# Kernel tuning notes

Measured on AMD Instinct MI355X. Metric: run time of the kernel, lower is better.

Reference implementation:

```python
import jax, jax.numpy as jnp
import numpy as np

B = 64       # number of graphs (regular batching)
NPER = 2048  # nodes per graph
K = 16       # kNN neighbors (includes self, as torch_cluster.knn does)
D_IN = 64
D_OUT = 64


def setup_inputs() -> dict:
    key = jax.random.key(0)
    k1, k2 = jax.random.split(key, 2)
    x = jax.random.normal(k1, (B * NPER, D_IN), jnp.float32)
    batch = jnp.repeat(jnp.arange(B, dtype=jnp.int32), NPER)
    # MLP: Linear(2*in_channels, out_channels, bias=True) + ReLU
    weight = jax.random.normal(k2, (D_OUT, 2 * D_IN), jnp.float32) * (1.0 / np.sqrt(2 * D_IN))
    bias = jnp.zeros((D_OUT,), jnp.float32)
    return {"x": x, "batch": batch, "weight": weight, "bias": bias}


def reference(x, batch, weight, bias):
    # batch is a regular assignment (NPER nodes per graph) -> block the kNN per graph
    d = x.shape[1]
    xb = x.reshape(B, NPER, d)                                   # [B, n, d]
    # squared euclidean distances within each graph
    sq = jnp.sum(xb * xb, axis=-1)                               # [B, n]
    dist = sq[:, :, None] + sq[:, None, :] - 2.0 * jnp.einsum('bnd,bmd->bnm', xb, xb)
    # k nearest (smallest distance); self-distance 0 -> self included, matching PyG knn
    _, idx = jax.lax.top_k(-dist, K)                             # [B, n, K]
    xj = jax.vmap(lambda feats, ids: feats[ids])(xb, idx)        # [B, n, K, d]
    xi = xb[:, :, None, :]                                        # [B, n, 1, d]
    msg = jnp.concatenate([jnp.broadcast_to(xi, xj.shape), xj - xi], axis=-1)  # [B,n,K,2d]
    h = jax.nn.relu(jnp.einsum('bnkf,of->bnko', msg, weight) + bias)
    out = jnp.max(h, axis=2)                                      # max aggregation over neighbors
    return out.reshape(B * NPER, -1)
```

## Files before the change

### kernel.cpp

```cpp
#include <hip/hip_runtime.h>
#include <cfloat>

#define BB 64
#define NPERB 2048
#define KNN 16
#define NTOT (BB*NPERB)
#define NCAND 24

typedef __bf16 bf16x8 __attribute__((ext_vector_type(8)));
typedef float  f32x4  __attribute__((ext_vector_type(4)));

__device__ __forceinline__ unsigned int med3u(unsigned int a, unsigned int b, unsigned int c) {
    unsigned int d;
    asm("v_med3_u32 %0, %1, %2, %3" : "=v"(d) : "v"(a), "v"(b), "v"(c));
    return d;
}

__device__ __forceinline__ float np_sq64(const float* __restrict__ xs) {
    float r[8];
#pragma unroll
    for (int j = 0; j < 8; ++j) r[j] = __fmul_rn(xs[j], xs[j]);
#pragma unroll
    for (int i = 1; i < 8; ++i)
#pragma unroll
        for (int j = 0; j < 8; ++j)
            r[j] = __fadd_rn(r[j], __fmul_rn(xs[8*i + j], xs[8*i + j]));
    float t01 = __fadd_rn(r[0], r[1]);
    float t23 = __fadd_rn(r[2], r[3]);
    float t45 = __fadd_rn(r[4], r[5]);
    float t67 = __fadd_rn(r[6], r[7]);
    return __fadd_rn(__fadd_rn(t01, t23), __fadd_rn(t45, t67));
}

__device__ __forceinline__ unsigned short bf16rn(float f) {
    unsigned int u = __float_as_uint(f);
    u += 0x7fffu + ((u >> 16) & 1u);
    return (unsigned short)(u >> 16);
}
__device__ __forceinline__ unsigned int pk2(float a, float b) {
    return ((unsigned int)bf16rn(b) << 16) | (unsigned int)bf16rn(a);
}

__global__ __launch_bounds__(256) void k_transform(const float* __restrict__ x,
    const float* __restrict__ w, const float* __restrict__ bias,
    float* __restrict__ Aout, float* __restrict__ Bvv, float* __restrict__ sqnp,
    unsigned int* __restrict__ xbu)
{
    __shared__ float w1m[64*64];
    __shared__ float w2t[64*64];
    __shared__ float xs[128*64];
    int t = threadIdx.x;
    int r0 = blockIdx.x * 128;
#pragma unroll
    for (int i = 0; i < 16; ++i) {
        int e = t + i*256; int f = e >> 6; int o = e & 63;
        float w2 = w[o*128 + 64 + f];
        float w1 = w[o*128 + f];
        w2t[f*64 + o] = w2;
        w1m[f*64 + o] = w1 - w2;
    }
#pragma unroll
    for (int i = 0; i < 32; ++i) { int idx = t + i*256; xs[idx] = x[(size_t)r0*64 + idx]; }
    __syncthreads();
#pragma unroll
    for (int i = 0; i < 16; ++i) {
        int e = t + i*256;
        xbu[(size_t)r0*32 + e] = pk2(xs[2*e], xs[2*e + 1]);
    }
    int o = t & 63;
    float br = bias[o];
    for (int g = 0; g < 32; ++g) {
        int rl = g*4 + (t >> 6);
        float a1 = 0.f, a2 = 0.f;
#pragma unroll
        for (int f = 0; f < 64; ++f) {
            float xv = xs[rl*64 + f];
            a1 += xv * w1m[f*64 + o];
            a2 += xv * w2t[f*64 + o];
        }
        int row = r0 + rl;
        Aout[(size_t)row*64 + o] = a1 + br;
        Bvv[(size_t)row*64 + o] = a2;
        if (o == 0) sqnp[row] = np_sq64(&xs[rl*64]);
    }
}

__global__ __launch_bounds__(256, 4) void k_topk(const float4* __restrict__ x4,
    const uint4* __restrict__ xb, const float* __restrict__ sq, int* __restrict__ nbr)
{
    __shared__ __align__(16) char smem[28160];
    unsigned short* bsh0 = (unsigned short*)smem;
    unsigned short* bsh1 = (unsigned short*)(smem + 9216);
    unsigned short* rsh  = (unsigned short*)(smem + 18432);
    float* sqc           = (float*)(smem + 27648);
    unsigned int* cand   = (unsigned int*)smem;
    unsigned short* cand24 = (unsigned short*)(smem + 17408);

    int t = threadIdx.x;
    int lane = t & 63;
    int w = t >> 6;
    int ln = lane & 15, qd = lane >> 4;
    int batch = blockIdx.x >> 5;
    int strip = blockIdx.x & 31;
    int rbase = batch * NPERB;
    int r0g = rbase + strip * 64;

    {
        const uint4* src = xb + (size_t)r0g * 8;
#pragma unroll
        for (int i = 0; i < 2; ++i) {
            int l = t + i*256;
            uint4 v = src[l];
            *(uint4*)&rsh[(l >> 3)*72 + (l & 7)*8] = v;
        }
    }
    uint4 pf0, pf1; float sqpf;
    {
        const uint4* src = xb + (size_t)rbase * 8;
        pf0 = src[t]; pf1 = src[t + 256];
        sqpf = (t < 64) ? sq[rbase + t] : 0.f;
    }
    __syncthreads();
    bf16x8 rf0 = *(const bf16x8*)&rsh[(w*16 + ln)*72 + qd*8];
    bf16x8 rf1 = *(const bf16x8*)&rsh[(w*16 + ln)*72 + 32 + qd*8];
    float sqr16 = sq[r0g + w*16 + ln] + 16.f;

    *(uint4*)&bsh0[(t >> 3)*72 + (t & 7)*8] = pf0;
    { int l1 = t + 256; *(uint4*)&bsh0[(l1 >> 3)*72 + (l1 & 7)*8] = pf1; }
    if (t < 64) sqc[t] = sqpf;
    {
        const uint4* src = xb + ((size_t)rbase + 64) * 8;
        pf0 = src[t]; pf1 = src[t + 256];
        sqpf = (t < 64) ? sq[rbase + 64 + t] : 0.f;
    }
    __syncthreads();

    unsigned int ks[16];
#pragma unroll
    for (int j = 0; j < 16; ++j) ks[j] = 0xFFFFFFFFu;

    for (int ct = 0; ct < 32; ++ct) {
        unsigned short* bcur = (ct & 1) ? bsh1 : bsh0;
        const float* sqcur = sqc + (ct & 1)*64;
#pragma unroll
        for (int ct2 = 0; ct2 < 4; ++ct2) {
            int pt = ct2*16 + ln;
            bf16x8 a0 = *(const bf16x8*)&bcur[pt*72 + qd*8];
            bf16x8 a1 = *(const bf16x8*)&bcur[pt*72 + 32 + qd*8];
            f32x4 acc = {0.f, 0.f, 0.f, 0.f};
            acc = __builtin_amdgcn_mfma_f32_16x16x32_bf16(a0, rf0, acc, 0, 0, 0);
            acc = __builtin_amdgcn_mfma_f32_16x16x32_bf16(a1, rf1, acc, 0, 0, 0);
            f32x4 sc4 = *(const f32x4*)&sqcur[ct2*16 + qd*4];
            int idxb = ct*64 + ct2*16 + qd*4;
#pragma unroll
            for (int j = 0; j < 4; ++j) {
                float s = fmaf(-2.f, acc[j], sc4[j] + sqr16);
                unsigned int u = (__float_as_uint(s) & 0xFFFFF800u) | (unsigned int)(idxb + j);
#pragma unroll
                for (int jj = 15; jj >= 1; --jj) ks[jj] = med3u(u, ks[jj-1], ks[jj]);
                ks[0] = min(ks[0], u);
            }
        }
        if (ct < 31) {
            unsigned short* bnext = (ct & 1) ? bsh0 : bsh1;
            *(uint4*)&bnext[(t >> 3)*72 + (t & 7)*8] = pf0;
            { int l1 = t + 256; *(uint4*)&bnext[(l1 >> 3)*72 + (l1 & 7)*8] = pf1; }
            if (t < 64) sqc[((ct + 1) & 1)*64 + t] = sqpf;
            if (ct < 30) {
                const uint4* src = xb + ((size_t)rbase + (ct + 2)*64) * 8;
                pf0 = src[t]; pf1 = src[t + 256];
                sqpf = (t < 64) ? sq[rbase + (ct + 2)*64 + t] : 0.f;
            }
        }
        __syncthreads();
    }

    {
        int r = w*16 + ln;
#pragma unroll
        for (int j = 0; j < 16; ++j) cand[r*68 + qd*16 + j] = ks[j];
    }
    __syncthreads();

    if (t < 64) {
        unsigned int m24[NCAND];
#pragma unroll
        for (int j = 0; j < NCAND; ++j) m24[j] = 0xFFFFFFFFu;
        for (int i = 0; i < 64; ++i) {
            unsigned int u = cand[t*68 + i];
#pragma unroll
            for (int jj = NCAND-1; jj >= 1; --jj) m24[jj] = med3u(u, m24[jj-1], m24[jj]);
            m24[0] = min(m24[0], u);
        }
#pragma unroll
        for (int j = 0; j < NCAND; ++j) cand24[t*NCAND + j] = (unsigned short)(m24[j] & 0x7FFu);
    }
    __syncthreads();

    {
        int r = t & 63, grp = t >> 6;
        float sqr = sq[r0g + r];
        float4 xrA[8];
#pragma unroll
        for (int i = 0; i < 8; ++i) xrA[i] = x4[(size_t)(r0g + r)*16 + i];
        float* kdf = (float*)cand;
#pragma unroll
        for (int m6 = 0; m6 < 6; ++m6) {
            int m = grp*6 + m6;
            int c = (int)cand24[r*NCAND + m];
            const float4* xb4 = &x4[(size_t)(rbase + c)*16];
            float dot = 0.f;
#pragma unroll
            for (int i = 0; i < 8; ++i) {
                float4 a = xrA[i]; float4 b = xb4[i];
                dot = fmaf(a.x, b.x, dot); dot = fmaf(a.y, b.y, dot);
                dot = fmaf(a.z, b.z, dot); dot = fmaf(a.w, b.w, dot);
            }
#pragma unroll
            for (int i = 8; i < 16; ++i) {
                float4 a = x4[(size_t)(r0g + r)*16 + i]; float4 b = xb4[i];
                dot = fmaf(a.x, b.x, dot); dot = fmaf(a.y, b.y, dot);
                dot = fmaf(a.z, b.z, dot); dot = fmaf(a.w, b.w, dot);
            }
            float kd = __fsub_rn(__fadd_rn(sqr, sq[rbase + c]), __fmul_rn(2.0f, dot));
            kdf[r*68 + m] = kd;
            cand[r*68 + 32 + m] = (unsigned int)c;
        }
    }
    __syncthreads();

    if (t < 64) {
        float* kdf = (float*)cand;
        float dk[KNN]; int di[KNN];
#pragma unroll
        for (int j = 0; j < KNN; ++j) { dk[j] = FLT_MAX; di[j] = 0x7fffffff; }
        for (int m = 0; m < NCAND; ++m) {
            float kd = kdf[t*68 + m];
            int c = (int)cand[t*68 + 32 + m];
            bool better = (kd < dk[KNN-1]) || (kd == dk[KNN-1] && c < di[KNN-1]);
            if (better) {
#pragma unroll
                for (int j = KNN-1; j >= 1; --j) {
                    bool sh = (dk[j-1] > kd) || (dk[j-1] == kd && di[j-1] > c);
                    bool pl = (!sh) && ((dk[j] > kd) || (dk[j] == kd && di[j] > c));
                    float nk = sh ? dk[j-1] : (pl ? kd : dk[j]);
                    int ni = sh ? di[j-1] : (pl ? c : di[j]);
                    dk[j] = nk; di[j] = ni;
                }
                if ((dk[0] > kd) || (dk[0] == kd && di[0] > c)) { dk[0] = kd; di[0] = c; }
            }
        }
#pragma unroll
        for (int k = 0; k < KNN; ++k) nbr[(size_t)(r0g + t)*16 + k] = di[k];
    }
}

__global__ __launch_bounds__(256) void k_combine(const float* __restrict__ Bvv,
    const int* __restrict__ nbr, float* __restrict__ out)
{
    int t = threadIdx.x;
    int row = blockIdx.x*4 + (t >> 6);
    int o = t & 63;
    int rb = (row >> 11) << 11;
    float m = -FLT_MAX;
#pragma unroll
    for (int k = 0; k < 16; ++k) {
        int c = nbr[(size_t)row*16 + k];
        m = fmaxf(m, Bvv[(size_t)(rb + c)*64 + o]);
    }
    out[(size_t)row*64 + o] = fmaxf(out[(size_t)row*64 + o] + m, 0.f);
}

extern "C" void kernel_launch(void* const* d_in, const int* in_sizes, int n_in,
                              void* d_out, int out_size, void* d_ws, size_t ws_size,
                              hipStream_t stream) {
    const float* x    = (const float*)d_in[0];
    const float* w    = (const float*)d_in[2];
    const float* bias = (const float*)d_in[3];
    float* out = (float*)d_out;

    float* Bvv  = (float*)d_ws;
    float* sqnp = Bvv + (size_t)NTOT * 64;
    int*   nbr  = (int*)(sqnp + NTOT);
    unsigned int* xbu = (unsigned int*)(nbr + (size_t)NTOT * 16);

    k_transform<<<1024, 256, 0, stream>>>(x, w, bias, out, Bvv, sqnp, xbu);
    k_topk<<<2048, 256, 0, stream>>>((const float4*)x, (const uint4*)xbu, sqnp, nbr);
    k_combine<<<NTOT/4, 256, 0, stream>>>(Bvv, nbr, out);
}
```

Before: 636.7 us.

## Process 128 query rows per topk block and vectorize transform weight reads

The kNN kernel now handles 128 query rows per block (two 16-row MFMA tiles per wave), so each staged candidate tile in shared memory is reused twice and the grid is halved. Query fragments are loaded straight from global memory instead of via shared memory, the candidate-merge stage runs in two halves, and refinement is spread over all 256 threads. Shared memory is trimmed and launch bounds raised to 5 blocks per SM. The transform kernel stores weights transposed with padding so the inner loop can use float4 LDS reads. The price is doubled register state for the two top-k lists, which may cause spills or lower occupancy.

After: 671.9 us. 5.5% more time.

```diff
diff --git a/kernel.cpp b/kernel.cpp
--- a/kernel.cpp
+++ b/kernel.cpp
@@ -46,18 +46,18 @@
     float* __restrict__ Aout, float* __restrict__ Bvv, float* __restrict__ sqnp,
     unsigned int* __restrict__ xbu)
 {
-    __shared__ float w1m[64*64];
-    __shared__ float w2t[64*64];
-    __shared__ float xs[128*64];
+    __shared__ __align__(16) float w1mT[64*68];
+    __shared__ __align__(16) float w2tT[64*68];
+    __shared__ __align__(16) float xs[128*64];
     int t = threadIdx.x;
     int r0 = blockIdx.x * 128;
 #pragma unroll
     for (int i = 0; i < 16; ++i) {
-        int e = t + i*256; int f = e >> 6; int o = e & 63;
+        int e = t + i*256; int o = e >> 6; int f = e & 63;
+        float w1 = w[o*128 + f];
         float w2 = w[o*128 + 64 + f];
-        float w1 = w[o*128 + f];
-        w2t[f*64 + o] = w2;
-        w1m[f*64 + o] = w1 - w2;
+        w1mT[o*68 + f] = w1 - w2;
+        w2tT[o*68 + f] = w2;
     }
 #pragma unroll
     for (int i = 0; i < 32; ++i) { int idx = t + i*256; xs[idx] = x[(size_t)r0*64 + idx]; }
@@ -68,15 +68,20 @@
         xbu[(size_t)r0*32 + e] = pk2(xs[2*e], xs[2*e + 1]);
     }
     int o = t & 63;
+    int rl0 = t >> 6;
     float br = bias[o];
     for (int g = 0; g < 32; ++g) {
-        int rl = g*4 + (t >> 6);
+        int rl = g*4 + rl0;
         float a1 = 0.f, a2 = 0.f;
 #pragma unroll
-        for (int f = 0; f < 64; ++f) {
-            float xv = xs[rl*64 + f];
-            a1 += xv * w1m[f*64 + o];
-            a2 += xv * w2t[f*64 + o];
+        for (int f4 = 0; f4 < 16; ++f4) {
+            float4 xv = *(const float4*)&xs[rl*64 + f4*4];
+            float4 wa = *(const float4*)&w1mT[o*68 + f4*4];
+            float4 wb = *(const float4*)&w2tT[o*68 + f4*4];
+            a1 = fmaf(xv.x, wa.x, a1); a1 = fmaf(xv.y, wa.y, a1);
+            a1 = fmaf(xv.z, wa.z, a1); a1 = fmaf(xv.w, wa.w, a1);
+            a2 = fmaf(xv.x, wb.x, a2); a2 = fmaf(xv.y, wb.y, a2);
+            a2 = fmaf(xv.z, wb.z, a2); a2 = fmaf(xv.w, wb.w, a2);
         }
         int row = r0 + rl;
         Aout[(size_t)row*64 + o] = a1 + br;
@@ -85,14 +90,13 @@
     }
 }
 
-__global__ __launch_bounds__(256, 4) void k_topk(const float4* __restrict__ x4,
-    const uint4* __restrict__ xb, const float* __restrict__ sq, int* __restrict__ nbr)
+__global__ __launch_bounds__(256, 5) void k_topk(const float4* __restrict__ x4,
+    const uint4* __restrict__ xbu, const float* __restrict__ sq, int* __restrict__ nbr)
 {
-    __shared__ __align__(16) char smem[28160];
+    __shared__ __align__(16) char smem[23552];
     unsigned short* bsh0 = (unsigned short*)smem;
     unsigned short* bsh1 = (unsigned short*)(smem + 9216);
-    unsigned short* rsh  = (unsigned short*)(smem + 18432);
-    float* sqc           = (float*)(smem + 27648);
+    float* sqc           = (float*)(smem + 18432);
     unsigned int* cand   = (unsigned int*)smem;
     unsigned short* cand24 = (unsigned short*)(smem + 17408);
 
@@ -100,44 +104,40 @@
     int lane = t & 63;
     int w = t >> 6;
     int ln = lane & 15, qd = lane >> 4;
-    int batch = blockIdx.x >> 5;
-    int strip = blockIdx.x & 31;
+    int batch = blockIdx.x >> 4;
+    int strip = blockIdx.x & 15;
     int rbase = batch * NPERB;
-    int r0g = rbase + strip * 64;
-
-    {
-        const uint4* src = xb + (size_t)r0g * 8;
-#pragma unroll
-        for (int i = 0; i < 2; ++i) {
-            int l = t + i*256;
-            uint4 v = src[l];
-            *(uint4*)&rsh[(l >> 3)*72 + (l & 7)*8] = v;
-        }
-    }
+    int r0g = rbase + strip * 128;
+
+    int rowA = r0g + w*32 + ln;
+    int rowB = rowA + 16;
+    bf16x8 rfA0, rfA1, rfB0, rfB1;
+    { uint4 v = xbu[(size_t)rowA*8 + qd];     rfA0 = *(bf16x8*)&v; }
+    { uint4 v = xbu[(size_t)rowA*8 + 4 + qd]; rfA1 = *(bf16x8*)&v; }
+    { uint4 v = xbu[(size_t)rowB*8 + qd];     rfB0 = *(bf16x8*)&v; }
+    { uint4 v = xbu[(size_t)rowB*8 + 4 + qd]; rfB1 = *(bf16x8*)&v; }
+    float sqr16A = sq[rowA] + 16.f;
+    float sqr16B = sq[rowB] + 16.f;
+
     uint4 pf0, pf1; float sqpf;
     {
-        const uint4* src = xb + (size_t)rbase * 8;
+        const uint4* src = xbu + (size_t)rbase * 8;
         pf0 = src[t]; pf1 = src[t + 256];
         sqpf = (t < 64) ? sq[rbase + t] : 0.f;
     }
-    __syncthreads();
-    bf16x8 rf0 = *(const bf16x8*)&rsh[(w*16 + ln)*72 + qd*8];
-    bf16x8 rf1 = *(const bf16x8*)&rsh[(w*16 + ln)*72 + 32 + qd*8];
-    float sqr16 = sq[r0g + w*16 + ln] + 16.f;
-
     *(uint4*)&bsh0[(t >> 3)*72 + (t & 7)*8] = pf0;
     { int l1 = t + 256; *(uint4*)&bsh0[(l1 >> 3)*72 + (l1 & 7)*8] = pf1; }
     if (t < 64) sqc[t] = sqpf;
     {
-        const uint4* src = xb + ((size_t)rbase + 64) * 8;
+        const uint4* src = xbu + ((size_t)rbase + 64) * 8;
         pf0 = src[t]; pf1 = src[t + 256];
         sqpf = (t < 64) ? sq[rbase + 64 + t] : 0.f;
     }
     __syncthreads();
 
-    unsigned int ks[16];
-#pragma unroll
-    for (int j = 0; j < 16; ++j) ks[j] = 0xFFFFFFFFu;
+    unsigned int ksA[16], ksB[16];
+#pragma unroll
+    for (int j = 0; j < 16; ++j) { ksA[j] = 0xFFFFFFFFu; ksB[j] = 0xFFFFFFFFu; }
 
     for (int ct = 0; ct < 32; ++ct) {
         unsigned short* bcur = (ct & 1) ? bsh1 : bsh0;
@@ -147,18 +147,26 @@
             int pt = ct2*16 + ln;
             bf16x8 a0 = *(const bf16x8*)&bcur[pt*72 + qd*8];
             bf16x8 a1 = *(const bf16x8*)&bcur[pt*72 + 32 + qd*8];
-            f32x4 acc = {0.f, 0.f, 0.f, 0.f};
-            acc = __builtin_amdgcn_mfma_f32_16x16x32_bf16(a0, rf0, acc, 0, 0, 0);
-            acc = __builtin_amdgcn_mfma_f32_16x16x32_bf16(a1, rf1, acc, 0, 0, 0);
+            f32x4 accA = {0.f, 0.f, 0.f, 0.f};
+            accA = __builtin_amdgcn_mfma_f32_16x16x32_bf16(a0, rfA0, accA, 0, 0, 0);
+            accA = __builtin_amdgcn_mfma_f32_16x16x32_bf16(a1, rfA1, accA, 0, 0, 0);
+            f32x4 accB = {0.f, 0.f, 0.f, 0.f};
+            accB = __builtin_amdgcn_mfma_f32_16x16x32_bf16(a0, rfB0, accB, 0, 0, 0);
+            accB = __builtin_amdgcn_mfma_f32_16x16x32_bf16(a1, rfB1, accB, 0, 0, 0);
             f32x4 sc4 = *(const f32x4*)&sqcur[ct2*16 + qd*4];
             int idxb = ct*64 + ct2*16 + qd*4;
 #pragma unroll
             for (int j = 0; j < 4; ++j) {
-                float s = fmaf(-2.f, acc[j], sc4[j] + sqr16);
-                unsigned int u = (__float_as_uint(s) & 0xFFFFF800u) | (unsigned int)(idxb + j);
-#pragma unroll
-                for (int jj = 15; jj >= 1; --jj) ks[jj] = med3u(u, ks[jj-1], ks[jj]);
-                ks[0] = min(ks[0], u);
+                float sA = fmaf(-2.f, accA[j], sc4[j] + sqr16A);
+                unsigned int uA = (__float_as_uint(sA) & 0xFFFFF800u) | (unsigned int)(idxb + j);
+#pragma unroll
+                for (int jj = 15; jj >= 1; --jj) ksA[jj] = med3u(uA, ksA[jj-1], ksA[jj]);
+                ksA[0] = min(ksA[0], uA);
+                float sB = fmaf(-2.f, accB[j], sc4[j] + sqr16B);
+                unsigned int uB = (__float_as_uint(sB) & 0xFFFFF800u) | (unsigned int)(idxb + j);
+#pragma unroll
+                for (int jj = 15; jj >= 1; --jj) ksB[jj] = med3u(uB, ksB[jj-1], ksB[jj]);
+                ksB[0] = min(ksB[0], uB);
             }
         }
         if (ct < 31) {
@@ -167,7 +175,7 @@
             { int l1 = t + 256; *(uint4*)&bnext[(l1 >> 3)*72 + (l1 & 7)*8] = pf1; }
             if (t < 64) sqc[((ct + 1) & 1)*64 + t] = sqpf;
             if (ct < 30) {
-                const uint4* src = xb + ((size_t)rbase + (ct + 2)*64) * 8;
+                const uint4* src = xbu + ((size_t)rbase + (ct + 2)*64) * 8;
                 pf0 = src[t]; pf1 = src[t + 256];
                 sqpf = (t < 64) ? sq[rbase + (ct + 2)*64 + t] : 0.f;
             }
@@ -175,38 +183,44 @@
         __syncthreads();
     }
 
+#pragma unroll
+    for (int h = 0; h < 2; ++h) {
+        if ((w >> 1) == h) {
+            int rlocA = (w & 1)*32 + ln;
+#pragma unroll
+            for (int j = 0; j < 16; ++j) cand[rlocA*68 + qd*16 + j] = ksA[j];
+#pragma unroll
+            for (int j = 0; j < 16; ++j) cand[(rlocA + 16)*68 + qd*16 + j] = ksB[j];
+        }
+        __syncthreads();
+        if (t < 64) {
+            unsigned int m24[NCAND];
+#pragma unroll
+            for (int j = 0; j < NCAND; ++j) m24[j] = 0xFFFFFFFFu;
+            for (int i = 0; i < 64; ++i) {
+                unsigned int u = cand[t*68 + i];
+#pragma unroll
+                for (int jj = NCAND-1; jj >= 1; --jj) m24[jj] = med3u(u, m24[jj-1], m24[jj]);
+                m24[0] = min(m24[0], u);
+            }
+#pragma unroll
+            for (int j = 0; j < NCAND; ++j)
+                cand24[(h*64 + t)*NCAND + j] = (unsigned short)(m24[j] & 0x7FFu);
+        }
+        __syncthreads();
+    }
+
     {
-        int r = w*16 + ln;
-#pragma unroll
-        for (int j = 0; j < 16; ++j) cand[r*68 + qd*16 + j] = ks[j];
-    }
-    __syncthreads();
-
-    if (t < 64) {
-        unsigned int m24[NCAND];
-#pragma unroll
-        for (int j = 0; j < NCAND; ++j) m24[j] = 0xFFFFFFFFu;
-        for (int i = 0; i < 64; ++i) {
-            unsigned int u = cand[t*68 + i];
-#pragma unroll
-            for (int jj = NCAND-1; jj >= 1; --jj) m24[jj] = med3u(u, m24[jj-1], m24[jj]);
-            m24[0] = min(m24[0], u);
-        }
-#pragma unroll
-        for (int j = 0; j < NCAND; ++j) cand24[t*NCAND + j] = (unsigned short)(m24[j] & 0x7FFu);
-    }
-    __syncthreads();
-
-    {
-        int r = t & 63, grp = t >> 6;
-        float sqr = sq[r0g + r];
+        int r = t & 127, half = t >> 7;
+        int gr = r0g + r;
+        float sqr = sq[gr];
         float4 xrA[8];
 #pragma unroll
-        for (int i = 0; i < 8; ++i) xrA[i] = x4[(size_t)(r0g + r)*16 + i];
+        for (int i = 0; i < 8; ++i) xrA[i] = x4[(size_t)gr*16 + i];
         float* kdf = (float*)cand;
 #pragma unroll
-        for (int m6 = 0; m6 < 6; ++m6) {
-            int m = grp*6 + m6;
+        for (int m12 = 0; m12 < 12; ++m12) {
+            int m = half*12 + m12;
             int c = (int)cand24[r*NCAND + m];
             const float4* xb4 = &x4[(size_t)(rbase + c)*16];
             float dot = 0.f;
@@ -218,25 +232,24 @@
             }
 #pragma unroll
             for (int i = 8; i < 16; ++i) {
-                float4 a = x4[(size_t)(r0g + r)*16 + i]; float4 b = xb4[i];
+                float4 a = x4[(size_t)gr*16 + i]; float4 b = xb4[i];
                 dot = fmaf(a.x, b.x, dot); dot = fmaf(a.y, b.y, dot);
                 dot = fmaf(a.z, b.z, dot); dot = fmaf(a.w, b.w, dot);
             }
             float kd = __fsub_rn(__fadd_rn(sqr, sq[rbase + c]), __fmul_rn(2.0f, dot));
-            kdf[r*68 + m] = kd;
-            cand[r*68 + 32 + m] = (unsigned int)c;
+            kdf[r*24 + m] = kd;
         }
     }
     __syncthreads();
 
-    if (t < 64) {
+    if (t < 128) {
         float* kdf = (float*)cand;
         float dk[KNN]; int di[KNN];
 #pragma unroll
         for (int j = 0; j < KNN; ++j) { dk[j] = FLT_MAX; di[j] = 0x7fffffff; }
         for (int m = 0; m < NCAND; ++m) {
-            float kd = kdf[t*68 + m];
-            int c = (int)cand[t*68 + 32 + m];
+            float kd = kdf[t*24 + m];
+            int c = (int)cand24[t*NCAND + m];
             bool better = (kd < dk[KNN-1]) || (kd == dk[KNN-1] && c < di[KNN-1]);
             if (better) {
 #pragma unroll
@@ -285,6 +298,6 @@
     unsigned int* xbu = (unsigned int*)(nbr + (size_t)NTOT * 16);
 
     k_transform<<<1024, 256, 0, stream>>>(x, w, bias, out, Bvv, sqnp, xbu);
-    k_topk<<<2048, 256, 0, stream>>>((const float4*)x, (const uint4*)xbu, sqnp, nbr);
+    k_topk<<<1024, 256, 0, stream>>>((const float4*)x, (const uint4*)xbu, sqnp, nbr);
     k_combine<<<NTOT/4, 256, 0, stream>>>(Bvv, nbr, out);
 }
```
